# Kernel tuning notes

Measured on AMD Instinct MI355X. Metric: run time of the kernel, lower is better.

Reference implementation:

```python
import jax, jax.numpy as jnp
import numpy as np

F_LEN = 21          # function_length
D_LEN = 41          # distribution_length
SLOPE = 1.0         # function_slope (nonzero -> tanh branch)
EPS = 1e-12         # torch F.normalize eps


def setup_inputs() -> dict:
    key = jax.random.key(0)
    k1, k2, k3, k4, k5 = jax.random.split(key, 5)
    B, L = 64, 2048
    S = F_LEN + D_LEN - 1  # 61, segment length required by the sliding slices
    lines_feature = jax.random.normal(k1, (B, L, 16), dtype=jnp.float32)
    pf = jax.random.uniform(k2, (B, L, S), dtype=jnp.float32, minval=0.1, maxval=1.0)
    pb = jax.random.uniform(k3, (B, L, S), dtype=jnp.float32, minval=0.1, maxval=1.0)
    slop = jax.random.uniform(k4, (B, L), dtype=jnp.float32, minval=0.5, maxval=2.5)
    amp = jax.random.uniform(k5, (B, L), dtype=jnp.float32, minval=0.1, maxval=0.4)
    return {
        "lines_feature": lines_feature,
        "lines_image_pf_segments": pf,
        "lines_image_pb_segments": pb,
        "lines_slop": slop,
        "lines_amplitude": amp,
    }


def reference(lines_feature, lines_image_pf_segments, lines_image_pb_segments,
              lines_slop, lines_amplitude):
    # lookup functions f/b over the function window  [B, L, F]
    x = jnp.arange(F_LEN, dtype=jnp.float32) - (F_LEN - 1) / 2.0
    lf = 0.5 - lines_amplitude[..., None] * jnp.tanh(x / (2.0 * lines_slop[..., None]))
    lb = 1.0 - lf

    # minimum variance floor (Laplace vs Gaussian)
    min_var_laplace = 1.0 / (2.0 * jnp.square(jnp.arctanh(2.0 * lines_amplitude)))
    min_var = jnp.maximum(min_var_laplace, lines_slop)

    # all D_LEN overlapping windows of length F_LEN, gathered in one shot
    idx = jnp.arange(D_LEN)[:, None] + jnp.arange(F_LEN)[None, :]   # [D, F]
    pf_win = lines_image_pf_segments[..., idx]                      # [B, L, D, F]
    pb_win = lines_image_pb_segments[..., idx]                      # [B, L, D, F]

    # log-domain product reduction over the window
    logp = jnp.log(pf_win * lf[..., None, :] + pb_win * lb[..., None, :]).sum(-1)
    dist = jnp.exp(logp)                                            # [B, L, D]

    # L1 normalize (torch.nn.functional.normalize, p=1)
    dist = dist / jnp.maximum(jnp.sum(jnp.abs(dist), axis=-1, keepdims=True), EPS)

    # line_distribution_extractor is identity pass-through of the distributions

    # Gaussian moment fit
    step = jnp.arange(D_LEN, dtype=jnp.float32)                     # [D]
    mean_tmp = jnp.sum(step * dist, axis=-1)                        # [B, L]
    var_tmp = jnp.sum(jnp.square(step - mean_tmp[..., None]) * dist, axis=-1)
    mean = mean_tmp - (D_LEN - 1) / 2.0
    var = jnp.maximum(var_tmp, min_var)
    return dist, mean, 1.0 / var
```

## Files before the change

kernel.cpp:

```cpp
#include <hip/hip_runtime.h>
#include <math.h>

#define F_LEN 21
#define D_LEN 41
#define S_LEN 61
#define ROWS 32
#define THREADS 256
#define NELEM (ROWS * S_LEN)
#define NV4   (NELEM / 4)
#define DOUT  (ROWS * D_LEN)
#define DV4   (DOUT / 4)

__global__ __launch_bounds__(THREADS, 4) void bp_kernel(
    const float* __restrict__ pf_g, const float* __restrict__ pb_g,
    const float* __restrict__ slop_g, const float* __restrict__ amp_g,
    float* __restrict__ out_dist, float* __restrict__ out_mean,
    float* __restrict__ out_ivar)
{
    __shared__ float2 lds_fb[NELEM];

    const int tid  = threadIdx.x;
    const int rl   = tid >> 3;
    const int q    = tid & 7;
    const int row0 = blockIdx.x * ROWS;
    const int r    = row0 + rl;

    const float4* pf4 = (const float4*)(pf_g + (size_t)row0 * S_LEN);
    const float4* pb4 = (const float4*)(pb_g + (size_t)row0 * S_LEN);
    #pragma unroll
    for (int it = 0; it < 2; ++it) {
        int idx4 = it * THREADS + tid;
        if (idx4 < NV4) {
            float4 f = pf4[idx4];
            float4 b = pb4[idx4];
            lds_fb[idx4 * 4 + 0] = make_float2(f.x, b.x);
            lds_fb[idx4 * 4 + 1] = make_float2(f.y, b.y);
            lds_fb[idx4 * 4 + 2] = make_float2(f.z, b.z);
            lds_fb[idx4 * 4 + 3] = make_float2(f.w, b.w);
        }
    }

    const float a  = amp_g[r];
    const float sl = slop_g[r];

    float lf[F_LEN];
    lf[10] = 0.5f;
    {
        const float E = __expf(1.0f / sl);
        float Ek = 1.0f;
        #pragma unroll
        for (int k = 1; k <= 10; ++k) {
            Ek *= E;
            float t = __fdividef(Ek - 1.0f, Ek + 1.0f);
            float dl = a * t;
            lf[10 + k] = 0.5f - dl;
            lf[10 - k] = 0.5f + dl;
        }
    }

    __syncthreads();

    const int  d0   = q * 5;
    const bool has6 = (q == 7);
    const int  base = rl * S_LEN + d0;

    float prod[6] = {1.0f, 1.0f, 1.0f, 1.0f, 1.0f, 1.0f};
    #pragma unroll
    for (int i = 0; i < 26; ++i) {
        float2 fb = lds_fb[base + i];
        float  df = fb.x - fb.y;
        #pragma unroll
        for (int dp = 0; dp < 6; ++dp) {
            const int j = i - dp;
            if (j >= 0 && j < F_LEN) {
                float t = fmaf(lf[j], df, fb.y);
                if (dp == 5) t = has6 ? t : 1.0f;
                prod[dp] *= t;
            }
        }
    }

    const float df0 = (float)d0;
    float s0 = 0.0f, s1 = 0.0f, s2 = 0.0f;
    #pragma unroll
    for (int dp = 0; dp < 6; ++dp) {
        float p = prod[dp];
        if (dp == 5) p = has6 ? p : 0.0f;
        float dv = df0 + (float)dp;
        s0 += p;
        s1 += dv * p;
        s2 += dv * dv * p;
    }
    #pragma unroll
    for (int w = 1; w < 8; w <<= 1) {
        s0 += __shfl_xor(s0, w, 64);
        s1 += __shfl_xor(s1, w, 64);
        s2 += __shfl_xor(s2, w, 64);
    }

    const float inv      = 1.0f / fmaxf(s0, 1e-12f);
    const float mean_tmp = s1 * inv;
    const float m2       = s2 * inv;
    const float var_tmp  = fmaf(-mean_tmp, mean_tmp, m2);

    const float two_a = 2.0f * a;
    const float at    = 0.5f * logf((1.0f + two_a) / (1.0f - two_a));
    const float min_v = fmaxf(0.5f / (at * at), sl);
    const float var   = fmaxf(var_tmp, min_v);

    if (q == 0) {
        out_mean[r] = mean_tmp - (float)((D_LEN - 1) / 2);
        out_ivar[r] = 1.0f / var;
    }

    __syncthreads();
    float* ldsd = (float*)lds_fb;
    #pragma unroll
    for (int dp = 0; dp < 5; ++dp)
        ldsd[rl * D_LEN + d0 + dp] = prod[dp] * inv;
    if (has6)
        ldsd[rl * D_LEN + 40] = prod[5] * inv;
    __syncthreads();

    const float4* ld4 = (const float4*)ldsd;
    float4* o4 = (float4*)(out_dist + (size_t)row0 * D_LEN);
    #pragma unroll
    for (int it = 0; it < 2; ++it) {
        int idx4 = it * THREADS + tid;
        if (idx4 < DV4) o4[idx4] = ld4[idx4];
    }
}

extern "C" void kernel_launch(void* const* d_in, const int* in_sizes, int n_in,
                              void* d_out, int out_size, void* d_ws, size_t ws_size,
                              hipStream_t stream) {
    const float* pf   = (const float*)d_in[1];
    const float* pb   = (const float*)d_in[2];
    const float* slop = (const float*)d_in[3];
    const float* amp  = (const float*)d_in[4];

    const int rows = in_sizes[3];

    float* out_dist = (float*)d_out;
    float* out_mean = out_dist + (size_t)rows * D_LEN;
    float* out_ivar = out_mean + rows;

    const int blocks = rows / ROWS;
    bp_kernel<<<blocks, THREADS, 0, stream>>>(pf, pb, slop, amp,
                                              out_dist, out_mean, out_ivar);
}
```

Before: 26.99 us.

## Shrink blocks to one wave, use DPP reductions and parallel power terms

Reduces block size from 256 threads/32 rows to 64 threads/8 rows, giving more, smaller workgroups and less LDS per block. Replaces shuffle-based 8-lane reductions with DPP quad_perm and row_half_mirror adds. Computes the tanh exponent powers with a shallow multiplication tree instead of a serial chain, and restricts the min-variance computation to one lane using a fast log. The fast log may slightly reduce accuracy, and many tiny blocks add scheduling overhead.

```diff
diff --git a/kernel.cpp b/kernel.cpp
--- a/kernel.cpp
+++ b/kernel.cpp
@@ -4,12 +4,21 @@
 #define F_LEN 21
 #define D_LEN 41
 #define S_LEN 61
-#define ROWS 32
-#define THREADS 256
+#define ROWS 8
+#define THREADS 64
 #define NELEM (ROWS * S_LEN)
 #define NV4   (NELEM / 4)
 #define DOUT  (ROWS * D_LEN)
 #define DV4   (DOUT / 4)
+
+template <int CTRL>
+__device__ __forceinline__ float dpp_add(float x) {
+    int y = __builtin_amdgcn_update_dpp(0, __float_as_int(x), CTRL, 0xf, 0xf, true);
+    return x + __int_as_float(y);
+}
+#define DPP_XOR1 0xB1
+#define DPP_XOR2 0x4E
+#define DPP_XOR7 0x141
 
 __global__ __launch_bounds__(THREADS, 4) void bp_kernel(
     const float* __restrict__ pf_g, const float* __restrict__ pb_g,
@@ -46,13 +55,19 @@
     float lf[F_LEN];
     lf[10] = 0.5f;
     {
-        const float E = __expf(1.0f / sl);
-        float Ek = 1.0f;
+        const float E1 = __expf(1.0f / sl);
+        const float E2 = E1 * E1;
+        const float E4 = E2 * E2;
+        const float E8 = E4 * E4;
+        float Ek[11];
+        Ek[1] = E1;        Ek[2] = E2;        Ek[3] = E2 * E1;
+        Ek[4] = E4;        Ek[5] = E4 * E1;   Ek[6] = E4 * E2;
+        Ek[7] = E4 * Ek[3];Ek[8] = E8;        Ek[9] = E8 * E1;
+        Ek[10] = E8 * E2;
         #pragma unroll
         for (int k = 1; k <= 10; ++k) {
-            Ek *= E;
-            float t = __fdividef(Ek - 1.0f, Ek + 1.0f);
-            float dl = a * t;
+            float rcp = __frcp_rn(Ek[k] + 1.0f);
+            float dl  = a * ((Ek[k] - 1.0f) * rcp);
             lf[10 + k] = 0.5f - dl;
             lf[10 - k] = 0.5f + dl;
         }
@@ -91,24 +106,20 @@
         s1 += dv * p;
         s2 += dv * dv * p;
     }
-    #pragma unroll
-    for (int w = 1; w < 8; w <<= 1) {
-        s0 += __shfl_xor(s0, w, 64);
-        s1 += __shfl_xor(s1, w, 64);
-        s2 += __shfl_xor(s2, w, 64);
-    }
+    s0 = dpp_add<DPP_XOR1>(s0); s0 = dpp_add<DPP_XOR2>(s0); s0 = dpp_add<DPP_XOR7>(s0);
+    s1 = dpp_add<DPP_XOR1>(s1); s1 = dpp_add<DPP_XOR2>(s1); s1 = dpp_add<DPP_XOR7>(s1);
+    s2 = dpp_add<DPP_XOR1>(s2); s2 = dpp_add<DPP_XOR2>(s2); s2 = dpp_add<DPP_XOR7>(s2);
 
     const float inv      = 1.0f / fmaxf(s0, 1e-12f);
     const float mean_tmp = s1 * inv;
     const float m2       = s2 * inv;
     const float var_tmp  = fmaf(-mean_tmp, mean_tmp, m2);
 
-    const float two_a = 2.0f * a;
-    const float at    = 0.5f * logf((1.0f + two_a) / (1.0f - two_a));
-    const float min_v = fmaxf(0.5f / (at * at), sl);
-    const float var   = fmaxf(var_tmp, min_v);
-
     if (q == 0) {
+        const float two_a = 2.0f * a;
+        const float at    = 0.5f * __logf((1.0f + two_a) / (1.0f - two_a));
+        const float min_v = fmaxf(0.5f / (at * at), sl);
+        const float var   = fmaxf(var_tmp, min_v);
         out_mean[r] = mean_tmp - (float)((D_LEN - 1) / 2);
         out_ivar[r] = 1.0f / var;
     }
```

New measurement: 26.90 us. About the same (-0.3%).
